# Performance work log

Hardware: AMD Instinct MI355X
Metric: run time of the kernel (lower is better)

The kernel has to match this reference:

```python
import jax, jax.numpy as jnp
import numpy as np

B, S, D, H = 2, 2048, 1024, 16
DK = D // H


def setup_inputs() -> dict:
    key = jax.random.key(0)
    ks = jax.random.split(key, 11)
    scale = 1.0 / np.sqrt(D)
    inp = {
        "Q": jax.random.normal(ks[0], (B, S, D), jnp.float32),
        "K": jax.random.normal(ks[1], (B, S, D), jnp.float32),
        "V": jax.random.normal(ks[2], (B, S, D), jnp.float32),
        # causal mask, shape (B, 1, S, S); 0 => masked
        "mask": jnp.broadcast_to(
            jnp.tril(jnp.ones((S, S), jnp.int32))[None, None], (B, 1, S, S)
        ),
        "Wq": jax.random.normal(ks[3], (D, D), jnp.float32) * scale,
        "bq": jnp.zeros((D,), jnp.float32),
        "Wk": jax.random.normal(ks[4], (D, D), jnp.float32) * scale,
        "bk": jnp.zeros((D,), jnp.float32),
        "Wv": jax.random.normal(ks[5], (D, D), jnp.float32) * scale,
        "bv": jnp.zeros((D,), jnp.float32),
        "Wo": jax.random.normal(ks[6], (D, D), jnp.float32) * scale,
        "bo": jnp.zeros((D,), jnp.float32),
    }
    return inp


def _split_heads(x):
    # (B, S, D) -> (B, H, S, DK)
    return x.reshape(B, S, H, DK).transpose(0, 2, 1, 3)


def reference(Q, K, V, mask, Wq, bq, Wk, bk, Wv, bv, Wo, bo):
    q = _split_heads(Q @ Wq.T + bq)
    k = _split_heads(K @ Wk.T + bk)
    v = _split_heads(V @ Wv.T + bv)
    scores = jnp.einsum("bhqd,bhkd->bhqk", q, k) / np.sqrt(DK)
    scores = jnp.where(mask == 0, -1e9, scores)
    probs = jax.nn.softmax(scores, axis=-1)
    attn = jnp.einsum("bhqk,bhkd->bhqd", probs, v)
    out = attn.transpose(0, 2, 1, 3).reshape(B, S, D)
    return out @ Wo.T + bo
```

## Files before the change

### kernel.cpp

```cpp
#include <hip/hip_runtime.h>
#include <hip/hip_bf16.h>

#define DEV static __device__ __forceinline__

typedef __attribute__((ext_vector_type(8))) short short8;
typedef __attribute__((ext_vector_type(4))) short short4v;
typedef __attribute__((ext_vector_type(4))) float f32x4;
typedef __attribute__((ext_vector_type(4))) float float4v;

constexpr int B_ = 2, S_ = 2048, D_ = 1024, H_ = 16, DK_ = 64;
constexpr int M_ = B_ * S_;

DEV short f2bf(float f) {
  unsigned u = __float_as_uint(f);
  u = u + 0x7FFF + ((u >> 16) & 1);
  return (short)(u >> 16);
}

#if __has_builtin(__builtin_amdgcn_exp2f)
DEV float fast_exp2(float x) { return __builtin_amdgcn_exp2f(x); }
#else
DEV float fast_exp2(float x) { return exp2f(x); }
#endif

#define GLOAD_LDS16(g, l)                                                      \
  __builtin_amdgcn_global_load_lds(                                            \
      (const __attribute__((address_space(1))) void*)(g),                      \
      (__attribute__((address_space(3))) void*)(l), 16, 0, 0)

__global__ __launch_bounds__(256) void cvt_f32_bf16(const float* __restrict__ src,
                                                    short* __restrict__ dst,
                                                    int n4) {
  int i = blockIdx.x * blockDim.x + threadIdx.x;
  const int stride = gridDim.x * blockDim.x;
  for (; i < n4; i += stride) {
    float4v f = ((const float4v*)src)[i];
    short4v o;
#pragma unroll
    for (int j = 0; j < 4; ++j) o[j] = f2bf(f[j]);
    ((short4v*)dst)[i] = o;
  }
}

template <int MODE>
__global__ __launch_bounds__(256) void gemm_proj(const short* __restrict__ A,
                                                 const short* __restrict__ Bt,
                                                 const float* __restrict__ bias,
                                                 void* __restrict__ dstv,
                                                 float scale) {
  constexpr int K = 1024;
  __shared__ short At[128 * 32];
  __shared__ short Bti[128 * 32];
  const int m0 = blockIdx.x * 128, n0 = blockIdx.y * 128;
  const int t = threadIdx.x;
  const int w = t >> 6, l = t & 63, lr = l & 15, lg = l >> 4;
  const int wm = w >> 1, wn = w & 1;

  f32x4 acc[4][4] = {};

  const int srow = t >> 2, scol = (t & 3) * 8;
  const short* gA = A + (m0 + srow) * K + scol;
  const short* gB = Bt + (n0 + srow) * K + scol;

  for (int k0 = 0; k0 < K; k0 += 32) {
    GLOAD_LDS16(gA + k0, At + t * 8);
    GLOAD_LDS16(gA + 64 * K + k0, At + 2048 + t * 8);
    GLOAD_LDS16(gB + k0, Bti + t * 8);
    GLOAD_LDS16(gB + 64 * K + k0, Bti + 2048 + t * 8);
    __syncthreads();
    short8 af[4], bfr[4];
#pragma unroll
    for (int mt = 0; mt < 4; ++mt)
      af[mt] = *(const short8*)&At[(wm * 64 + mt * 16 + lr) * 32 + lg * 8];
#pragma unroll
    for (int nt = 0; nt < 4; ++nt)
      bfr[nt] = *(const short8*)&Bti[(wn * 64 + nt * 16 + lr) * 32 + lg * 8];
#pragma unroll
    for (int mt = 0; mt < 4; ++mt)
#pragma unroll
      for (int nt = 0; nt < 4; ++nt)
        acc[mt][nt] = __builtin_amdgcn_mfma_f32_16x16x32_bf16(
            af[mt], bfr[nt], acc[mt][nt], 0, 0, 0);
    __syncthreads();
  }

#pragma unroll
  for (int mt = 0; mt < 4; ++mt) {
#pragma unroll
    for (int nt = 0; nt < 4; ++nt) {
      const int n = n0 + wn * 64 + nt * 16 + lr;
      const float bn = bias[n];
#pragma unroll
      for (int r = 0; r < 4; ++r) {
        const int m = m0 + wm * 64 + mt * 16 + lg * 4 + r;
        const float v = (acc[mt][nt][r] + bn) * scale;
        if (MODE == 0) {
          const int b = m >> 11, s = m & 2047, h = n >> 6, dk = n & 63;
          ((short*)dstv)[(((b * 16 + h) * 2048) + s) * 64 + dk] = f2bf(v);
        } else if (MODE == 1) {
          const int b = m >> 11, s = m & 2047, h = n >> 6, dk = n & 63;
          ((short*)dstv)[(((b * 16 + h) * 64) + dk) * 2048 + s] = f2bf(v);
        } else {
          ((float*)dstv)[m * 1024 + n] = v;
        }
      }
    }
  }
}

__global__ __launch_bounds__(256) void attn_kernel(const short* __restrict__ q,
                                                   const short* __restrict__ k,
                                                   const short* __restrict__ vt,
                                                   short* __restrict__ attn) {
  constexpr int S = 2048, DK = 64;
  const int qb = blockIdx.x;
  const int bh = blockIdx.y;
  const int t = threadIdx.x;
  const int w = t >> 6, l = t & 63, lr = l & 15, lg = l >> 4;

  const short* qh = q + bh * S * DK;
  const short* kh = k + bh * S * DK;
  const short* vth = vt + bh * DK * S;

  __shared__ short Pl[4 * 1024];
  char* Pw = (char*)(Pl + w * 1024);

  const int qrow = qb * 64 + w * 16;

  short8 aq[2];
  aq[0] = *(const short8*)&qh[(qrow + lr) * DK + lg * 8];
  aq[1] = *(const short8*)&qh[(qrow + lr) * DK + 32 + lg * 8];

  f32x4 o[4] = {};
  float mrun[4], lrun[4];
#pragma unroll
  for (int r = 0; r < 4; ++r) { mrun[r] = -1e30f; lrun[r] = 0.f; }

  for (int kb = 0; kb <= qb; ++kb) {
    const int kbase = kb * 64;
    f32x4 s[4] = {};
#pragma unroll
    for (int tt = 0; tt < 4; ++tt) {
      short8 bk0 = *(const short8*)&kh[(kbase + tt * 16 + lr) * DK + lg * 8];
      short8 bk1 = *(const short8*)&kh[(kbase + tt * 16 + lr) * DK + 32 + lg * 8];
      s[tt] = __builtin_amdgcn_mfma_f32_16x16x32_bf16(aq[0], bk0, s[tt], 0, 0, 0);
      s[tt] = __builtin_amdgcn_mfma_f32_16x16x32_bf16(aq[1], bk1, s[tt], 0, 0, 0);
    }
    if (kb == qb) {
#pragma unroll
      for (int tt = 0; tt < 4; ++tt)
#pragma unroll
        for (int r = 0; r < 4; ++r) {
          const int key = kbase + tt * 16 + lr;
          const int qr = qrow + lg * 4 + r;
          if (key > qr) s[tt][r] = -1e30f;
        }
    }
    float mnew[4], fac[4];
#pragma unroll
    for (int r = 0; r < 4; ++r) {
      float pm = fmaxf(fmaxf(s[0][r], s[1][r]), fmaxf(s[2][r], s[3][r]));
#pragma unroll
      for (int msk = 1; msk < 16; msk <<= 1) pm = fmaxf(pm, __shfl_xor(pm, msk));
      mnew[r] = fmaxf(mrun[r], pm);
      fac[r] = fast_exp2((mrun[r] - mnew[r]) * 1.44269504f);
      mrun[r] = mnew[r];
    }
#pragma unroll
    for (int tt = 0; tt < 4; ++tt)
#pragma unroll
      for (int r = 0; r < 4; ++r)
        s[tt][r] = fast_exp2((s[tt][r] - mnew[r]) * 1.44269504f);
#pragma unroll
    for (int r = 0; r < 4; ++r) {
      float sum = s[0][r] + s[1][r] + s[2][r] + s[3][r];
#pragma unroll
      for (int msk = 1; msk < 16; msk <<= 1) sum += __shfl_xor(sum, msk);
      lrun[r] = lrun[r] * fac[r] + sum;
    }
#pragma unroll
    for (int dt = 0; dt < 4; ++dt)
#pragma unroll
      for (int r = 0; r < 4; ++r) o[dt][r] *= fac[r];

#pragma unroll
    for (int tt = 0; tt < 4; ++tt)
#pragma unroll
      for (int r = 0; r < 4; ++r) {
        const int row = lg * 4 + r, col = tt * 16 + lr;
        int byte = row * 128 + col * 2;
        byte ^= (row & 7) << 4;
        *(short*)(Pw + byte) = f2bf(s[tt][r]);
      }
    short8 pa[2];
#pragma unroll
    for (int c2 = 0; c2 < 2; ++c2) {
      int byte = lr * 128 + c2 * 64 + lg * 16;
      byte ^= (lr & 7) << 4;
      pa[c2] = *(const short8*)(Pw + byte);
    }
#pragma unroll
    for (int c2 = 0; c2 < 2; ++c2)
#pragma unroll
      for (int dt = 0; dt < 4; ++dt) {
        short8 bv = *(const short8*)&vth[(dt * 16 + lr) * S + kbase + c2 * 32 + lg * 8];
        o[dt] = __builtin_amdgcn_mfma_f32_16x16x32_bf16(pa[c2], bv, o[dt], 0, 0, 0);
      }
  }

  float inv[4];
#pragma unroll
  for (int r = 0; r < 4; ++r) inv[r] = 1.0f / lrun[r];
  const int b = bh >> 4, h = bh & 15;
#pragma unroll
  for (int dt = 0; dt < 4; ++dt)
#pragma unroll
    for (int r = 0; r < 4; ++r) {
      const int sm = qrow + lg * 4 + r;
      attn[(b * 2048 + sm) * 1024 + h * 64 + dt * 16 + lr] = f2bf(o[dt][r] * inv[r]);
    }
}

extern "C" void kernel_launch(void* const* d_in, const int* in_sizes, int n_in,
                              void* d_out, int out_size, void* d_ws, size_t ws_size,
                              hipStream_t stream) {
  const float* Q = (const float*)d_in[0];
  const float* K = (const float*)d_in[1];
  const float* V = (const float*)d_in[2];
  const float* Wq = (const float*)d_in[4];
  const float* bq = (const float*)d_in[5];
  const float* Wk = (const float*)d_in[6];
  const float* bk = (const float*)d_in[7];
  const float* Wv = (const float*)d_in[8];
  const float* bv = (const float*)d_in[9];
  const float* Wo = (const float*)d_in[10];
  const float* bo = (const float*)d_in[11];

  char* ws = (char*)d_ws;
  short* Qb  = (short*)(ws);
  short* Kb  = (short*)(ws + (8u << 20));
  short* Vb  = (short*)(ws + (16u << 20));
  short* Wqb = (short*)(ws + (24u << 20));
  short* Wkb = (short*)(ws + (26u << 20));
  short* Wvb = (short*)(ws + (28u << 20));
  short* Wob = (short*)(ws + (30u << 20));
  short* qp  = (short*)(ws + (32u << 20));
  short* kp  = (short*)(ws + (40u << 20));
  short* vtp = (short*)(ws + (48u << 20));
  short* attn = Qb;

  const int TPB = 256;
  const int nQKV4 = (B_ * S_ * D_) / 4;
  const int nW4 = (D_ * D_) / 4;

  cvt_f32_bf16<<<1024, TPB, 0, stream>>>(Q, Qb, nQKV4);
  cvt_f32_bf16<<<1024, TPB, 0, stream>>>(K, Kb, nQKV4);
  cvt_f32_bf16<<<1024, TPB, 0, stream>>>(V, Vb, nQKV4);
  cvt_f32_bf16<<<512, TPB, 0, stream>>>(Wq, Wqb, nW4);
  cvt_f32_bf16<<<512, TPB, 0, stream>>>(Wk, Wkb, nW4);
  cvt_f32_bf16<<<512, TPB, 0, stream>>>(Wv, Wvb, nW4);
  cvt_f32_bf16<<<512, TPB, 0, stream>>>(Wo, Wob, nW4);

  dim3 ggrid(M_ / 128, D_ / 128);
  gemm_proj<0><<<ggrid, TPB, 0, stream>>>(Qb, Wqb, bq, qp, 0.125f);
  gemm_proj<0><<<ggrid, TPB, 0, stream>>>(Kb, Wkb, bk, kp, 1.0f);
  gemm_proj<1><<<ggrid, TPB, 0, stream>>>(Vb, Wvb, bv, vtp, 1.0f);

  attn_kernel<<<dim3(S_ / 64, B_ * H_), TPB, 0, stream>>>(qp, kp, vtp, attn);

  gemm_proj<2><<<ggrid, TPB, 0, stream>>>(attn, Wob, bo, d_out, 1.0f);
}
```

Before: 525.0 us.

## Batch conversions, shrink GEMM N tile, prefetch K/V and cheapen softmax in attention

The seven f32→bf16 conversion launches become two batched launches. The projection GEMM N tile is halved from 128 to 64, doubling the grid for occupancy. The V-transpose row stride is padded to 2176 to avoid channel or bank conflicts. In the attention loop, K tiles are register double-buffered and V fragments are loaded before the softmax. The log2(e) factor is folded into the Q scale, the row-sum shuffle reduction is deferred to the end, and the max reduction uses DPP instead of shuffles. Together these aim to cut launch overhead, memory latency stalls and ALU work, at the cost of higher register pressure and smaller GEMM tiles with less reuse.

```diff
diff --git a/kernel.cpp b/kernel.cpp
--- a/kernel.cpp
+++ b/kernel.cpp
@@ -10,6 +10,7 @@
 
 constexpr int B_ = 2, S_ = 2048, D_ = 1024, H_ = 16, DK_ = 64;
 constexpr int M_ = B_ * S_;
+constexpr int VS_ = 2176;
 
 DEV short f2bf(float f) {
   unsigned u = __float_as_uint(f);
@@ -17,20 +18,36 @@
   return (short)(u >> 16);
 }
 
-#if __has_builtin(__builtin_amdgcn_exp2f)
 DEV float fast_exp2(float x) { return __builtin_amdgcn_exp2f(x); }
-#else
-DEV float fast_exp2(float x) { return exp2f(x); }
-#endif
+
+#define DPPMAXS(x, c)                                                          \
+  x = fmaxf(x, __int_as_float(__builtin_amdgcn_update_dpp(                     \
+             __float_as_int(x), __float_as_int(x), c, 0xF, 0xF, false)))
+#define DPPSUMS(x, c)                                                          \
+  x = x + __int_as_float(__builtin_amdgcn_update_dpp(                          \
+             __float_as_int(x), __float_as_int(x), c, 0xF, 0xF, false))
+
+DEV float red16_max(float x) {
+  DPPMAXS(x, 0xB1);
+  DPPMAXS(x, 0x4E);
+  DPPMAXS(x, 0x124);
+  DPPMAXS(x, 0x128);
+  return x;
+}
+DEV float red16_sum(float x) {
+  DPPSUMS(x, 0xB1);
+  DPPSUMS(x, 0x4E);
+  DPPSUMS(x, 0x124);
+  DPPSUMS(x, 0x128);
+  return x;
+}
 
 #define GLOAD_LDS16(g, l)                                                      \
   __builtin_amdgcn_global_load_lds(                                            \
       (const __attribute__((address_space(1))) void*)(g),                      \
       (__attribute__((address_space(3))) void*)(l), 16, 0, 0)
 
-__global__ __launch_bounds__(256) void cvt_f32_bf16(const float* __restrict__ src,
-                                                    short* __restrict__ dst,
-                                                    int n4) {
+DEV void cvt_loop(const float* __restrict__ src, short* __restrict__ dst, int n4) {
   int i = blockIdx.x * blockDim.x + threadIdx.x;
   const int stride = gridDim.x * blockDim.x;
   for (; i < n4; i += stride) {
@@ -40,6 +57,25 @@
     for (int j = 0; j < 4; ++j) o[j] = f2bf(f[j]);
     ((short4v*)dst)[i] = o;
   }
+}
+
+__global__ __launch_bounds__(256) void cvt3(const float* a, const float* b,
+                                            const float* c, short* da, short* db,
+                                            short* dc, int n4) {
+  const float* s = (blockIdx.y == 0) ? a : (blockIdx.y == 1) ? b : c;
+  short* d = (blockIdx.y == 0) ? da : (blockIdx.y == 1) ? db : dc;
+  cvt_loop(s, d, n4);
+}
+
+__global__ __launch_bounds__(256) void cvt4(const float* a, const float* b,
+                                            const float* c, const float* e,
+                                            short* da, short* db, short* dc,
+                                            short* de, int n4) {
+  const float* s = (blockIdx.y == 0) ? a : (blockIdx.y == 1) ? b
+                   : (blockIdx.y == 2) ? c : e;
+  short* d = (blockIdx.y == 0) ? da : (blockIdx.y == 1) ? db
+             : (blockIdx.y == 2) ? dc : de;
+  cvt_loop(s, d, n4);
 }
 
 template <int MODE>
@@ -50,13 +86,13 @@
                                                  float scale) {
   constexpr int K = 1024;
   __shared__ short At[128 * 32];
-  __shared__ short Bti[128 * 32];
-  const int m0 = blockIdx.x * 128, n0 = blockIdx.y * 128;
+  __shared__ short Bti[64 * 32];
+  const int m0 = blockIdx.x * 128, n0 = blockIdx.y * 64;
   const int t = threadIdx.x;
   const int w = t >> 6, l = t & 63, lr = l & 15, lg = l >> 4;
   const int wm = w >> 1, wn = w & 1;
 
-  f32x4 acc[4][4] = {};
+  f32x4 acc[4][2] = {};
 
   const int srow = t >> 2, scol = (t & 3) * 8;
   const short* gA = A + (m0 + srow) * K + scol;
@@ -66,19 +102,18 @@
     GLOAD_LDS16(gA + k0, At + t * 8);
     GLOAD_LDS16(gA + 64 * K + k0, At + 2048 + t * 8);
     GLOAD_LDS16(gB + k0, Bti + t * 8);
-    GLOAD_LDS16(gB + 64 * K + k0, Bti + 2048 + t * 8);
     __syncthreads();
-    short8 af[4], bfr[4];
+    short8 af[4], bfr[2];
 #pragma unroll
     for (int mt = 0; mt < 4; ++mt)
       af[mt] = *(const short8*)&At[(wm * 64 + mt * 16 + lr) * 32 + lg * 8];
 #pragma unroll
-    for (int nt = 0; nt < 4; ++nt)
-      bfr[nt] = *(const short8*)&Bti[(wn * 64 + nt * 16 + lr) * 32 + lg * 8];
+    for (int nt = 0; nt < 2; ++nt)
+      bfr[nt] = *(const short8*)&Bti[(wn * 32 + nt * 16 + lr) * 32 + lg * 8];
 #pragma unroll
     for (int mt = 0; mt < 4; ++mt)
 #pragma unroll
-      for (int nt = 0; nt < 4; ++nt)
+      for (int nt = 0; nt < 2; ++nt)
         acc[mt][nt] = __builtin_amdgcn_mfma_f32_16x16x32_bf16(
             af[mt], bfr[nt], acc[mt][nt], 0, 0, 0);
     __syncthreads();
@@ -87,8 +122,8 @@
 #pragma unroll
   for (int mt = 0; mt < 4; ++mt) {
 #pragma unroll
-    for (int nt = 0; nt < 4; ++nt) {
-      const int n = n0 + wn * 64 + nt * 16 + lr;
+    for (int nt = 0; nt < 2; ++nt) {
+      const int n = n0 + wn * 32 + nt * 16 + lr;
       const float bn = bias[n];
 #pragma unroll
       for (int r = 0; r < 4; ++r) {
@@ -99,7 +134,7 @@
           ((short*)dstv)[(((b * 16 + h) * 2048) + s) * 64 + dk] = f2bf(v);
         } else if (MODE == 1) {
           const int b = m >> 11, s = m & 2047, h = n >> 6, dk = n & 63;
-          ((short*)dstv)[(((b * 16 + h) * 64) + dk) * 2048 + s] = f2bf(v);
+          ((short*)dstv)[(((b * 16 + h) * 64) + dk) * VS_ + s] = f2bf(v);
         } else {
           ((float*)dstv)[m * 1024 + n] = v;
         }
@@ -120,7 +155,7 @@
 
   const short* qh = q + bh * S * DK;
   const short* kh = k + bh * S * DK;
-  const short* vth = vt + bh * DK * S;
+  const short* vth = vt + (long)bh * DK * VS_;
 
   __shared__ short Pl[4 * 1024];
   char* Pw = (char*)(Pl + w * 1024);
@@ -132,20 +167,42 @@
   aq[1] = *(const short8*)&qh[(qrow + lr) * DK + 32 + lg * 8];
 
   f32x4 o[4] = {};
-  float mrun[4], lrun[4];
-#pragma unroll
-  for (int r = 0; r < 4; ++r) { mrun[r] = -1e30f; lrun[r] = 0.f; }
+  float mrun[4], lsum[4];
+#pragma unroll
+  for (int r = 0; r < 4; ++r) { mrun[r] = -1e30f; lsum[r] = 0.f; }
+
+  short8 bk0[4], bk1[4], nk0[4], nk1[4];
+#pragma unroll
+  for (int tt = 0; tt < 4; ++tt) {
+    bk0[tt] = *(const short8*)&kh[(tt * 16 + lr) * DK + lg * 8];
+    bk1[tt] = *(const short8*)&kh[(tt * 16 + lr) * DK + 32 + lg * 8];
+  }
 
   for (int kb = 0; kb <= qb; ++kb) {
     const int kbase = kb * 64;
-    f32x4 s[4] = {};
+    f32x4 s4[4] = {};
 #pragma unroll
     for (int tt = 0; tt < 4; ++tt) {
-      short8 bk0 = *(const short8*)&kh[(kbase + tt * 16 + lr) * DK + lg * 8];
-      short8 bk1 = *(const short8*)&kh[(kbase + tt * 16 + lr) * DK + 32 + lg * 8];
-      s[tt] = __builtin_amdgcn_mfma_f32_16x16x32_bf16(aq[0], bk0, s[tt], 0, 0, 0);
-      s[tt] = __builtin_amdgcn_mfma_f32_16x16x32_bf16(aq[1], bk1, s[tt], 0, 0, 0);
-    }
+      s4[tt] = __builtin_amdgcn_mfma_f32_16x16x32_bf16(aq[0], bk0[tt], s4[tt], 0, 0, 0);
+      s4[tt] = __builtin_amdgcn_mfma_f32_16x16x32_bf16(aq[1], bk1[tt], s4[tt], 0, 0, 0);
+    }
+    const bool more = (kb < qb);
+    if (more) {
+      const short* knx = kh + (kbase + 64) * DK;
+#pragma unroll
+      for (int tt = 0; tt < 4; ++tt) {
+        nk0[tt] = *(const short8*)&knx[(tt * 16 + lr) * DK + lg * 8];
+        nk1[tt] = *(const short8*)&knx[(tt * 16 + lr) * DK + 32 + lg * 8];
+      }
+    }
+    short8 bv[8];
+#pragma unroll
+    for (int c2 = 0; c2 < 2; ++c2)
+#pragma unroll
+      for (int dt = 0; dt < 4; ++dt)
+        bv[c2 * 4 + dt] =
+            *(const short8*)&vth[(dt * 16 + lr) * VS_ + kbase + c2 * 32 + lg * 8];
+
     if (kb == qb) {
 #pragma unroll
       for (int tt = 0; tt < 4; ++tt)
@@ -153,31 +210,26 @@
         for (int r = 0; r < 4; ++r) {
           const int key = kbase + tt * 16 + lr;
           const int qr = qrow + lg * 4 + r;
-          if (key > qr) s[tt][r] = -1e30f;
+          if (key > qr) s4[tt][r] = -1e30f;
         }
     }
     float mnew[4], fac[4];
 #pragma unroll
     for (int r = 0; r < 4; ++r) {
-      float pm = fmaxf(fmaxf(s[0][r], s[1][r]), fmaxf(s[2][r], s[3][r]));
-#pragma unroll
-      for (int msk = 1; msk < 16; msk <<= 1) pm = fmaxf(pm, __shfl_xor(pm, msk));
+      float pm = fmaxf(fmaxf(s4[0][r], s4[1][r]), fmaxf(s4[2][r], s4[3][r]));
+      pm = red16_max(pm);
       mnew[r] = fmaxf(mrun[r], pm);
-      fac[r] = fast_exp2((mrun[r] - mnew[r]) * 1.44269504f);
+      fac[r] = fast_exp2(mrun[r] - mnew[r]);
       mrun[r] = mnew[r];
     }
 #pragma unroll
     for (int tt = 0; tt < 4; ++tt)
 #pragma unroll
       for (int r = 0; r < 4; ++r)
-        s[tt][r] = fast_exp2((s[tt][r] - mnew[r]) * 1.44269504f);
-#pragma unroll
-    for (int r = 0; r < 4; ++r) {
-      float sum = s[0][r] + s[1][r] + s[2][r] + s[3][r];
-#pragma unroll
-      for (int msk = 1; msk < 16; msk <<= 1) sum += __shfl_xor(sum, msk);
-      lrun[r] = lrun[r] * fac[r] + sum;
-    }
+        s4[tt][r] = fast_exp2(s4[tt][r] - mnew[r]);
+#pragma unroll
+    for (int r = 0; r < 4; ++r)
+      lsum[r] = lsum[r] * fac[r] + (s4[0][r] + s4[1][r] + s4[2][r] + s4[3][r]);
 #pragma unroll
     for (int dt = 0; dt < 4; ++dt)
 #pragma unroll
@@ -190,7 +242,7 @@
         const int row = lg * 4 + r, col = tt * 16 + lr;
         int byte = row * 128 + col * 2;
         byte ^= (row & 7) << 4;
-        *(short*)(Pw + byte) = f2bf(s[tt][r]);
+        *(short*)(Pw + byte) = f2bf(s4[tt][r]);
       }
     short8 pa[2];
 #pragma unroll
@@ -202,15 +254,18 @@
 #pragma unroll
     for (int c2 = 0; c2 < 2; ++c2)
 #pragma unroll
-      for (int dt = 0; dt < 4; ++dt) {
-        short8 bv = *(const short8*)&vth[(dt * 16 + lr) * S + kbase + c2 * 32 + lg * 8];
-        o[dt] = __builtin_amdgcn_mfma_f32_16x16x32_bf16(pa[c2], bv, o[dt], 0, 0, 0);
-      }
+      for (int dt = 0; dt < 4; ++dt)
+        o[dt] = __builtin_amdgcn_mfma_f32_16x16x32_bf16(pa[c2], bv[c2 * 4 + dt],
+                                                        o[dt], 0, 0, 0);
+    if (more) {
+#pragma unroll
+      for (int tt = 0; tt < 4; ++tt) { bk0[tt] = nk0[tt]; bk1[tt] = nk1[tt]; }
+    }
   }
 
   float inv[4];
 #pragma unroll
-  for (int r = 0; r < 4; ++r) inv[r] = 1.0f / lrun[r];
+  for (int r = 0; r < 4; ++r) inv[r] = 1.0f / red16_sum(lsum[r]);
   const int b = bh >> 4, h = bh & 15;
 #pragma unroll
   for (int dt = 0; dt < 4; ++dt)
@@ -246,27 +301,22 @@
   short* Wob = (short*)(ws + (30u << 20));
   short* qp  = (short*)(ws + (32u << 20));
   short* kp  = (short*)(ws + (40u << 20));
-  short* vtp = (short*)(ws + (48u << 20));
-  short* attn = Qb;
+  short* vtp = (short*)(ws);
+  short* attnout = Vb;
 
   const int TPB = 256;
   const int nQKV4 = (B_ * S_ * D_) / 4;
   const int nW4 = (D_ * D_) / 4;
 
-  cvt_f32_bf16<<<1024, TPB, 0, stream>>>(Q, Qb, nQKV4);
-  cvt_f32_bf16<<<1024, TPB, 0, stream>>>(K, Kb, nQKV4);
-  cvt_f32_bf16<<<1024, TPB, 0, stream>>>(V, Vb, nQKV4);
-  cvt_f32_bf16<<<512, TPB, 0, stream>>>(Wq, Wqb, nW4);
-  cvt_f32_bf16<<<512, TPB, 0, stream>>>(Wk, Wkb, nW4);
-  cvt_f32_bf16<<<512, TPB, 0, stream>>>(Wv, Wvb, nW4);
-  cvt_f32_bf16<<<512, TPB, 0, stream>>>(Wo, Wob, nW4);
-
-  dim3 ggrid(M_ / 128, D_ / 128);
-  gemm_proj<0><<<ggrid, TPB, 0, stream>>>(Qb, Wqb, bq, qp, 0.125f);
+  cvt3<<<dim3(512, 3), TPB, 0, stream>>>(Q, K, V, Qb, Kb, Vb, nQKV4);
+  cvt4<<<dim3(128, 4), TPB, 0, stream>>>(Wq, Wk, Wv, Wo, Wqb, Wkb, Wvb, Wob, nW4);
+
+  dim3 ggrid(M_ / 128, D_ / 64);
+  gemm_proj<0><<<ggrid, TPB, 0, stream>>>(Qb, Wqb, bq, qp, 0.18033688f);
   gemm_proj<0><<<ggrid, TPB, 0, stream>>>(Kb, Wkb, bk, kp, 1.0f);
   gemm_proj<1><<<ggrid, TPB, 0, stream>>>(Vb, Wvb, bv, vtp, 1.0f);
 
-  attn_kernel<<<dim3(S_ / 64, B_ * H_), TPB, 0, stream>>>(qp, kp, vtp, attn);
-
-  gemm_proj<2><<<ggrid, TPB, 0, stream>>>(attn, Wob, bo, d_out, 1.0f);
-}
+  attn_kernel<<<dim3(S_ / 64, B_ * H_), TPB, 0, stream>>>(qp, kp, vtp, attnout);
+
+  gemm_proj<2><<<ggrid, TPB, 0, stream>>>(attnout, Wob, bo, d_out, 1.0f);
+}
```

Result: faster. 448.5 us (-14.6%).
